# Kernel tuning notes

Hardware: AMD Instinct MI355X
Metric: run time of the kernel (lower is better)

Reference implementation:

```python
import jax, jax.numpy as jnp
import numpy as np

BATCH, SEQ, DIM = 16, 512, 2048
KEEP_RATIO = 0.75
TARGET_LEN = int(SEQ * KEEP_RATIO)      # 384
NUM_PAIRS = SEQ - TARGET_LEN            # 128 greedy merges
IMP_FLOOR = 0.1                          # max(0.1, importance) as in source


def gelu(x):
    return jax.nn.gelu(x, approximate=False)  # torch nn.GELU default (erf)


def setup_inputs() -> dict:
    key = jax.random.key(0)
    ks = jax.random.split(key, 6)
    s = 0.02
    return {
        "x": jax.random.normal(ks[0], (BATCH, SEQ, DIM), jnp.float32),
        # importance_scorer: Linear(dim, dim//2) -> GELU -> Linear(dim//2, 1) -> Sigmoid
        "imp_w1": (jax.random.normal(ks[1], (DIM, DIM // 2), jnp.float32) * s),
        "imp_b1": jnp.zeros((DIM // 2,), jnp.float32),
        "imp_w2": (jax.random.normal(ks[2], (DIM // 2, 1), jnp.float32) * s),
        "imp_b2": jnp.zeros((1,), jnp.float32),
        # token_merger: Linear(2*dim, dim) -> GELU -> Linear(dim, dim)
        "mrg_w1": (jax.random.normal(ks[3], (2 * DIM, DIM), jnp.float32) * s),
        "mrg_b1": jnp.zeros((DIM,), jnp.float32),
        "mrg_w2": (jax.random.normal(ks[4], (DIM, DIM), jnp.float32) * s),
        "mrg_b2": jnp.zeros((DIM,), jnp.float32),
    }


def importance_scores(x, w1, b1, w2, b2):
    # [B,S,1] sigmoid scores, then per-batch global min-max normalization
    imp = jax.nn.sigmoid(gelu(x @ w1 + b1) @ w2 + b2)
    mn = imp.min(axis=(1, 2), keepdims=True)
    mx = imp.max(axis=(1, 2), keepdims=True)
    return jnp.where(mx > mn, (imp - mn) / (mx - mn), imp)


def combined_scores(x, imp):
    # cosine similarity with diagonal = -1, divided by importance products
    xn = x / jnp.maximum(jnp.linalg.norm(x, axis=-1, keepdims=True), 1e-12)
    sim = jnp.einsum("bsd,btd->bst", xn, xn)
    w = jnp.maximum(imp[..., 0], IMP_FLOOR)                 # [B,S]
    eye = jnp.eye(SEQ, dtype=bool)
    return jnp.where(eye[None], -1.0, sim / (w[:, :, None] * w[:, None, :]))


def greedy_pairs(score):
    # Device-side greedy max-selection with suppression (NMS-style):
    # repeatedly pick the global argmax among rows/cols not yet merged.
    S = score.shape[0]

    def step(t, carry):
        avail, pi, pj = carry
        m = avail[:, None] & avail[None, :]
        flat = jnp.where(m, score, -jnp.inf).reshape(-1)
        idx = jnp.argmax(flat)
        i = (idx // S).astype(jnp.int32)
        j = (idx % S).astype(jnp.int32)
        avail = avail.at[i].set(False).at[j].set(False)
        return avail, pi.at[t].set(i), pj.at[t].set(j)

    init = (jnp.ones((S,), bool),
            jnp.zeros((NUM_PAIRS,), jnp.int32),
            jnp.zeros((NUM_PAIRS,), jnp.int32))
    return jax.lax.fori_loop(0, NUM_PAIRS, step, init)


def reference(x, imp_w1, imp_b1, imp_w2, imp_b2, mrg_w1, mrg_b1, mrg_w2, mrg_b2):
    B, S, D = x.shape
    imp = importance_scores(x, imp_w1, imp_b1, imp_w2, imp_b2)   # [B,S,1]
    score = combined_scores(x, imp)                              # [B,S,S]
    avail, pi, pj = jax.vmap(greedy_pairs)(score)                # [B,S],[B,P],[B,P]

    xi = jnp.take_along_axis(x, pi[:, :, None], axis=1)          # [B,P,D]
    xj = jnp.take_along_axis(x, pj[:, :, None], axis=1)          # [B,P,D]
    pair = jnp.concatenate([xi, xj], axis=-1)                    # [B,P,2D]
    merged = gelu(pair @ mrg_w1 + mrg_b1) @ mrg_w2 + mrg_b2      # [B,P,D]

    # unmerged tokens, ascending original order (fixed count S - 2P)
    un = jnp.sort(jnp.where(avail, jnp.arange(S)[None, :], S), axis=1)[:, : S - 2 * NUM_PAIRS]
    xu = jnp.take_along_axis(x, un[:, :, None], axis=1)          # [B,S-2P,D]

    return jnp.concatenate([merged, xu], axis=1)                 # [B,S-P,D]
```

## Files before the change

### kernel.cpp

```cpp
#include <hip/hip_runtime.h>
#include <math.h>

#define BATCH 16
#define SEQ 512
#define DIM 2048
#define HID 1024
#define NPAIRS 128
#define TLEN 384
#define NUN 256

typedef unsigned long long ull;
typedef short bf16x8 __attribute__((ext_vector_type(8)));
typedef float f32x4 __attribute__((ext_vector_type(4)));
typedef double f64x4 __attribute__((ext_vector_type(4)));

__device__ __forceinline__ unsigned short f2bf(float f) {
  unsigned u = __float_as_uint(f);
  unsigned r = (u + 0x7FFFu + ((u >> 16) & 1u)) >> 16;
  return (unsigned short)r;
}

__global__ __launch_bounds__(64)
void cc_probe_f64(int* __restrict__ flag) {
  __shared__ double Af[16][4];
  __shared__ double Bf[4][16];
  int l = threadIdx.x;
  if (l < 16)
#pragma unroll
    for (int k = 0; k < 4; ++k) {
      Af[l][k] = 1.0 + (double)l + 16.0 * k;
      Bf[k][l] = 2.0 + 3.0 * (double)l + 5.0 * k;
    }
  __syncthreads();
  int lr = l & 15, lk = l >> 4;
  double a = Af[lr][lk];
  double b = Bf[lk][lr];
  f64x4 d = {0.0, 0.0, 0.0, 0.0};
  d = __builtin_amdgcn_mfma_f64_16x16x4f64(a, b, d, 0, 0, 0);
  int best = 255;
  for (int H = 0; H < 4; ++H) {
    bool ok = true;
#pragma unroll
    for (int v = 0; v < 4; ++v) {
      int r, c;
      if (H == 0)      { r = 4 * lk + v; c = lr; }
      else if (H == 1) { r = lr; c = 4 * lk + v; }
      else if (H == 2) { r = lk + 4 * v; c = lr; }
      else             { r = lr; c = lk + 4 * v; }
      double tr = 0.0;
#pragma unroll
      for (int k = 0; k < 4; ++k) tr += Af[r][k] * Bf[k][c];
      if (d[v] != tr) ok = false;
    }
    ull m = __ballot(ok);
    if (m == ~0ull) { best = H; break; }
  }
  if (l == 0) *flag = best;
}

__global__ __launch_bounds__(256)
void cc_gemm_h(const float* __restrict__ A, const float* __restrict__ Bw,
               const float* __restrict__ bias, float* __restrict__ C,
               const int* __restrict__ flagp) {
  const int N = HID, K = DIM;
  __shared__ double As[16][66];
  __shared__ double Bs[16][66];
  const int H = *flagp;
  int tid = threadIdx.x;
  int lane = tid & 63, wave = tid >> 6;
  int wr = wave >> 1, wc = wave & 1;
  int lr = lane & 15, lk = lane >> 4;
  int pr[4], pc[4];
#pragma unroll
  for (int v = 0; v < 4; ++v) {
    if (H == 0)      { pr[v] = 4 * lk + v; pc[v] = lr; }
    else if (H == 1) { pr[v] = lr; pc[v] = 4 * lk + v; }
    else if (H == 2) { pr[v] = lk + 4 * v; pc[v] = lr; }
    else             { pr[v] = lr; pc[v] = lk + 4 * v; }
  }
  int tx = tid % 16, ty = tid / 16;
  int m0 = blockIdx.y * 64, n0 = blockIdx.x * 64;
  f64x4 acc[2][2] = {{{0.,0.,0.,0.},{0.,0.,0.,0.}},{{0.,0.,0.,0.},{0.,0.,0.,0.}}};
  double vacc[4][4] = {};
  for (int k0 = 0; k0 < K; k0 += 16) {
#pragma unroll
    for (int u = 0; u < 4; ++u) {
      int l = tid + u * 256;
      int r = l >> 4, k = l & 15;
      As[k][r] = (double)A[(size_t)(m0 + r) * K + k0 + k];
      int kb = l >> 6, n = l & 63;
      Bs[kb][n] = (double)Bw[(size_t)(k0 + kb) * N + n0 + n];
    }
    __syncthreads();
    if (H < 4) {
#pragma unroll
      for (int k4 = 0; k4 < 4; ++k4) {
        int kk = k4 * 4 + lk;
        double a0 = As[kk][wr * 32 + lr];
        double a1 = As[kk][wr * 32 + 16 + lr];
        double b0 = Bs[kk][wc * 32 + lr];
        double b1 = Bs[kk][wc * 32 + 16 + lr];
        acc[0][0] = __builtin_amdgcn_mfma_f64_16x16x4f64(a0, b0, acc[0][0], 0, 0, 0);
        acc[0][1] = __builtin_amdgcn_mfma_f64_16x16x4f64(a0, b1, acc[0][1], 0, 0, 0);
        acc[1][0] = __builtin_amdgcn_mfma_f64_16x16x4f64(a1, b0, acc[1][0], 0, 0, 0);
        acc[1][1] = __builtin_amdgcn_mfma_f64_16x16x4f64(a1, b1, acc[1][1], 0, 0, 0);
      }
    } else {
#pragma unroll
      for (int k = 0; k < 16; ++k) {
        double a0 = As[k][ty * 4 + 0], a1 = As[k][ty * 4 + 1];
        double a2 = As[k][ty * 4 + 2], a3 = As[k][ty * 4 + 3];
        double b0 = Bs[k][tx * 4 + 0], b1 = Bs[k][tx * 4 + 1];
        double b2 = Bs[k][tx * 4 + 2], b3 = Bs[k][tx * 4 + 3];
        vacc[0][0] = fma(a0, b0, vacc[0][0]); vacc[0][1] = fma(a0, b1, vacc[0][1]);
        vacc[0][2] = fma(a0, b2, vacc[0][2]); vacc[0][3] = fma(a0, b3, vacc[0][3]);
        vacc[1][0] = fma(a1, b0, vacc[1][0]); vacc[1][1] = fma(a1, b1, vacc[1][1]);
        vacc[1][2] = fma(a1, b2, vacc[1][2]); vacc[1][3] = fma(a1, b3, vacc[1][3]);
        vacc[2][0] = fma(a2, b0, vacc[2][0]); vacc[2][1] = fma(a2, b1, vacc[2][1]);
        vacc[2][2] = fma(a2, b2, vacc[2][2]); vacc[2][3] = fma(a2, b3, vacc[2][3]);
        vacc[3][0] = fma(a3, b0, vacc[3][0]); vacc[3][1] = fma(a3, b1, vacc[3][1]);
        vacc[3][2] = fma(a3, b2, vacc[3][2]); vacc[3][3] = fma(a3, b3, vacc[3][3]);
      }
    }
    __syncthreads();
  }
  if (H < 4) {
#pragma unroll
    for (int i = 0; i < 2; ++i)
#pragma unroll
      for (int j = 0; j < 2; ++j)
#pragma unroll
        for (int v = 0; v < 4; ++v) {
          int m = m0 + wr * 32 + i * 16 + pr[v];
          int n = n0 + wc * 32 + j * 16 + pc[v];
          float pre = (float)(acc[i][j][v] + (double)bias[n]);
          double vv = (double)pre;
          double g = 0.5 * vv * (1.0 + erf(vv * 0.70710678118654752440));
          C[(size_t)m * N + n] = (float)g;
        }
  } else {
#pragma unroll
    for (int i = 0; i < 4; ++i)
#pragma unroll
      for (int j = 0; j < 4; ++j) {
        int m = m0 + ty * 4 + i, n = n0 + tx * 4 + j;
        float pre = (float)(vacc[i][j] + (double)bias[n]);
        double vv = (double)pre;
        double g = 0.5 * vv * (1.0 + erf(vv * 0.70710678118654752440));
        C[(size_t)m * N + n] = (float)g;
      }
  }
}

__global__ __launch_bounds__(256)
void cc_imp2(const float* __restrict__ h, const float* __restrict__ w2,
             const float* __restrict__ b2, float* __restrict__ imp) {
  int row = blockIdx.x, tid = threadIdx.x;
  __shared__ double red[256];
  double s = 0.0;
  const float* hr = h + (size_t)row * HID;
  for (int k = tid; k < HID; k += 256) s = fma((double)hr[k], (double)w2[k], s);
  red[tid] = s;
  __syncthreads();
  for (int off = 128; off > 0; off >>= 1) {
    if (tid < off) red[tid] += red[tid + off];
    __syncthreads();
  }
  if (tid == 0) {
    float logit = (float)(red[0] + (double)b2[0]);
    double sg = 1.0 / (1.0 + exp(-(double)logit));
    imp[row] = (float)sg;
  }
}

__global__ __launch_bounds__(512)
void cc_minmax(const float* __restrict__ imp, float* __restrict__ w) {
  int b = blockIdx.x, tid = threadIdx.x;
  __shared__ float mn[512], mx[512];
  float v = imp[b * SEQ + tid];
  mn[tid] = v; mx[tid] = v;
  __syncthreads();
  for (int off = 256; off > 0; off >>= 1) {
    if (tid < off) {
      mn[tid] = fminf(mn[tid], mn[tid + off]);
      mx[tid] = fmaxf(mx[tid], mx[tid + off]);
    }
    __syncthreads();
  }
  float lo = mn[0], hi = mx[0];
  float nv = (hi > lo) ? (v - lo) / (hi - lo) : v;
  w[b * SEQ + tid] = fmaxf(nv, 0.1f);
}

__global__ __launch_bounds__(256)
void cc_rownorm(const float* __restrict__ x, float* __restrict__ rn) {
  int row = blockIdx.x, tid = threadIdx.x;
  __shared__ double red[256];
  double s = 0.0;
  const float* xr = x + (size_t)row * DIM;
  for (int k = tid; k < DIM; k += 256) {
    double v = xr[k];
    s = fma(v, v, s);
  }
  red[tid] = s;
  __syncthreads();
  for (int off = 128; off > 0; off >>= 1) {
    if (tid < off) red[tid] += red[tid + off];
    __syncthreads();
  }
  if (tid == 0) rn[row] = fmaxf((float)sqrt(red[0]), 1e-12f);
}

__global__ __launch_bounds__(256)
void cc_gemm_score(const float* __restrict__ X, const float* __restrict__ rn,
                   const float* __restrict__ w, float* __restrict__ score,
                   const int* __restrict__ flagp) {
  const int b = blockIdx.z;
  __shared__ double As[16][66];
  __shared__ double Bs[16][66];
  const int H = *flagp;
  int tid = threadIdx.x;
  int lane = tid & 63, wave = tid >> 6;
  int wr = wave >> 1, wc = wave & 1;
  int lr = lane & 15, lk = lane >> 4;
  int pr[4], pc[4];
#pragma unroll
  for (int v = 0; v < 4; ++v) {
    if (H == 0)      { pr[v] = 4 * lk + v; pc[v] = lr; }
    else if (H == 1) { pr[v] = lr; pc[v] = 4 * lk + v; }
    else if (H == 2) { pr[v] = lk + 4 * v; pc[v] = lr; }
    else             { pr[v] = lr; pc[v] = lk + 4 * v; }
  }
  int tx = tid % 16, ty = tid / 16;
  int s0 = blockIdx.y * 64, t0 = blockIdx.x * 64;
  const float* Xb = X + (size_t)b * SEQ * DIM;
  const float* rnb = rn + b * SEQ;
  f64x4 acc[2][2] = {{{0.,0.,0.,0.},{0.,0.,0.,0.}},{{0.,0.,0.,0.},{0.,0.,0.,0.}}};
  double vacc[4][4] = {};
  for (int k0 = 0; k0 < DIM; k0 += 16) {
#pragma unroll
    for (int u = 0; u < 4; ++u) {
      int l = tid + u * 256;
      int r = l >> 4, k = l & 15;
      As[k][r] = (double)(Xb[(size_t)(s0 + r) * DIM + k0 + k] / rnb[s0 + r]);
      Bs[k][r] = (double)(Xb[(size_t)(t0 + r) * DIM + k0 + k] / rnb[t0 + r]);
    }
    __syncthreads();
    if (H < 4) {
#pragma unroll
      for (int k4 = 0; k4 < 4; ++k4) {
        int kk = k4 * 4 + lk;
        double a0 = As[kk][wr * 32 + lr];
        double a1 = As[kk][wr * 32 + 16 + lr];
        double b0 = Bs[kk][wc * 32 + lr];
        double b1 = Bs[kk][wc * 32 + 16 + lr];
        acc[0][0] = __builtin_amdgcn_mfma_f64_16x16x4f64(a0, b0, acc[0][0], 0, 0, 0);
        acc[0][1] = __builtin_amdgcn_mfma_f64_16x16x4f64(a0, b1, acc[0][1], 0, 0, 0);
        acc[1][0] = __builtin_amdgcn_mfma_f64_16x16x4f64(a1, b0, acc[1][0], 0, 0, 0);
        acc[1][1] = __builtin_amdgcn_mfma_f64_16x16x4f64(a1, b1, acc[1][1], 0, 0, 0);
      }
    } else {
#pragma unroll
      for (int k = 0; k < 16; ++k) {
        double a0 = As[k][ty * 4 + 0], a1 = As[k][ty * 4 + 1];
        double a2 = As[k][ty * 4 + 2], a3 = As[k][ty * 4 + 3];
        double b0 = Bs[k][tx * 4 + 0], b1 = Bs[k][tx * 4 + 1];
        double b2 = Bs[k][tx * 4 + 2], b3 = Bs[k][tx * 4 + 3];
        vacc[0][0] = fma(a0, b0, vacc[0][0]); vacc[0][1] = fma(a0, b1, vacc[0][1]);
        vacc[0][2] = fma(a0, b2, vacc[0][2]); vacc[0][3] = fma(a0, b3, vacc[0][3]);
        vacc[1][0] = fma(a1, b0, vacc[1][0]); vacc[1][1] = fma(a1, b1, vacc[1][1]);
        vacc[1][2] = fma(a1, b2, vacc[1][2]); vacc[1][3] = fma(a1, b3, vacc[1][3]);
        vacc[2][0] = fma(a2, b0, vacc[2][0]); vacc[2][1] = fma(a2, b1, vacc[2][1]);
        vacc[2][2] = fma(a2, b2, vacc[2][2]); vacc[2][3] = fma(a2, b3, vacc[2][3]);
        vacc[3][0] = fma(a3, b0, vacc[3][0]); vacc[3][1] = fma(a3, b1, vacc[3][1]);
        vacc[3][2] = fma(a3, b2, vacc[3][2]); vacc[3][3] = fma(a3, b3, vacc[3][3]);
      }
    }
    __syncthreads();
  }
  if (H < 4) {
#pragma unroll
    for (int i = 0; i < 2; ++i)
#pragma unroll
      for (int j = 0; j < 2; ++j)
#pragma unroll
        for (int v = 0; v < 4; ++v) {
          int s = s0 + wr * 32 + i * 16 + pr[v];
          int t = t0 + wc * 32 + j * 16 + pc[v];
          float vv;
          if (s == t) vv = -1.0f;
          else {
            float sim = (float)acc[i][j][v];
            float wp = w[b * SEQ + s] * w[b * SEQ + t];
            vv = sim / wp;
          }
          score[((size_t)b * SEQ + s) * SEQ + t] = vv;
        }
  } else {
#pragma unroll
    for (int i = 0; i < 4; ++i)
#pragma unroll
      for (int j = 0; j < 4; ++j) {
        int s = s0 + ty * 4 + i, t = t0 + tx * 4 + j;
        float vv;
        if (s == t) vv = -1.0f;
        else {
          float sim = (float)vacc[i][j];
          float wp = w[b * SEQ + s] * w[b * SEQ + t];
          vv = sim / wp;
        }
        score[((size_t)b * SEQ + s) * SEQ + t] = vv;
      }
  }
}

__global__ __launch_bounds__(64)
void cc_greedy(const float* __restrict__ score, int* __restrict__ pi,
               int* __restrict__ pj, unsigned char* __restrict__ availg) {
  const int b = blockIdx.x;
  const float* S = score + (size_t)b * SEQ * SEQ;
  const int lane = threadIdx.x;
  __shared__ uint2 availv[SEQ / 8];
  unsigned char* avail = (unsigned char*)availv;
  __shared__ int rargL[SEQ];
  __shared__ int spi[NPAIRS], spj[NPAIRS];
  unsigned rhi8[8];
  int rarg8[8];
  unsigned am = 0xFFu;

  availv[lane] = make_uint2(0x01010101u, 0x01010101u);

  {
    float bv[8]; int bc[8];
#pragma unroll
    for (int q = 0; q < 8; ++q) { bv[q] = -INFINITY; bc[q] = 0; }
    for (int c4 = 0; c4 < SEQ / 4; ++c4) {
#pragma unroll
      for (int q = 0; q < 8; ++q) {
        int r = lane * 8 + q;
        float4 v = ((const float4*)(S + (size_t)r * SEQ))[c4];
        int cc = c4 * 4;
        if (v.x > bv[q]) { bv[q] = v.x; bc[q] = cc; }
        if (v.y > bv[q]) { bv[q] = v.y; bc[q] = cc + 1; }
        if (v.z > bv[q]) { bv[q] = v.z; bc[q] = cc + 2; }
        if (v.w > bv[q]) { bv[q] = v.w; bc[q] = cc + 3; }
      }
    }
#pragma unroll
    for (int q = 0; q < 8; ++q) {
      unsigned u = __float_as_uint(bv[q]);
      rhi8[q] = (u & 0x80000000u) ? ~u : (u | 0x80000000u);
      rarg8[q] = bc[q];
      rargL[lane * 8 + q] = bc[q];
    }
  }
  __syncthreads();

  for (int t = 0; t < NPAIRS; ++t) {
    ull key = 0ULL;
#pragma unroll
    for (int q = 0; q < 8; ++q) {
      if (am & (1u << q)) {
        ull k = ((ull)rhi8[q] << 32) | (unsigned)((SEQ - 1) - (lane * 8 + q));
        if (k > key) key = k;
      }
    }
#pragma unroll
    for (int off = 1; off < 64; off <<= 1) {
      ull ok = __shfl_xor(key, off, 64);
      if (ok > key) key = ok;
    }
    const int i = (SEQ - 1) - (int)(key & 0xFFFFFFFFull);
    const int j = rargL[i];
    if (lane == 0) {
      spi[t] = i; spj[t] = j;
      avail[i] = 0; avail[j] = 0;
    }
    if ((i >> 3) == lane) am &= ~(1u << (i & 7));
    if ((j >> 3) == lane) am &= ~(1u << (j & 7));
    __syncthreads();

    unsigned needmask = 0u;
#pragma unroll
    for (int q = 0; q < 8; ++q)
      if ((am & (1u << q)) && (rarg8[q] == i || rarg8[q] == j))
        needmask |= (1u << q);
    for (int q = 0; q < 8; ++q) {
      ull m = __ballot((needmask >> q) & 1u);
      while (m) {
        int src = __ffsll(m) - 1;
        m &= m - 1;
        int r = src * 8 + q;
        const float4* row4 = (const float4*)(S + (size_t)r * SEQ) + lane * 2;
        float4 v0 = row4[0], v1 = row4[1];
        uint2 av = availv[lane];
        float nv = -INFINITY; int nc = -1;
        if ((av.x & 0x000000FFu) && v0.x > nv) { nv = v0.x; nc = 0; }
        if ((av.x & 0x0000FF00u) && v0.y > nv) { nv = v0.y; nc = 1; }
        if ((av.x & 0x00FF0000u) && v0.z > nv) { nv = v0.z; nc = 2; }
        if ((av.x & 0xFF000000u) && v0.w > nv) { nv = v0.w; nc = 3; }
        if ((av.y & 0x000000FFu) && v1.x > nv) { nv = v1.x; nc = 4; }
        if ((av.y & 0x0000FF00u) && v1.y > nv) { nv = v1.y; nc = 5; }
        if ((av.y & 0x00FF0000u) && v1.z > nv) { nv = v1.z; nc = 6; }
        if ((av.y & 0xFF000000u) && v1.w > nv) { nv = v1.w; nc = 7; }
        ull rk = 0ULL;
        if (nc >= 0) {
          unsigned u = __float_as_uint(nv);
          unsigned ou = (u & 0x80000000u) ? ~u : (u | 0x80000000u);
          rk = ((ull)ou << 32) | (unsigned)((SEQ - 1) - (lane * 8 + nc));
        }
#pragma unroll
        for (int off = 1; off < 64; off <<= 1) {
          ull ok = __shfl_xor(rk, off, 64);
          if (ok > rk) rk = ok;
        }
        if (lane == src) {
          rhi8[q] = (unsigned)(rk >> 32);
          rarg8[q] = (SEQ - 1) - (int)(rk & 0xFFFFFFFFull);
          rargL[r] = rarg8[q];
        }
      }
    }
    __syncthreads();
  }

  for (int t2 = lane; t2 < NPAIRS; t2 += 64) {
    pi[b * NPAIRS + t2] = spi[t2];
    pj[b * NPAIRS + t2] = spj[t2];
  }
#pragma unroll
  for (int q = 0; q < 8; ++q) {
    int r = lane * 8 + q;
    availg[b * SEQ + r] = avail[r];
  }
}

__global__ __launch_bounds__(512)
void cc_unmerged(const unsigned char* __restrict__ availg, int* __restrict__ un) {
  int b = blockIdx.x, tid = threadIdx.x;
  __shared__ int ps[SEQ];
  int flag = availg[b * SEQ + tid];
  ps[tid] = flag;
  __syncthreads();
  for (int off = 1; off < SEQ; off <<= 1) {
    int v = (tid >= off) ? ps[tid - off] : 0;
    __syncthreads();
    ps[tid] += v;
    __syncthreads();
  }
  int pos = ps[tid] - flag;
  if (flag && pos < NUN) un[b * NUN + pos] = tid;
}

__global__ __launch_bounds__(256)
void cc_unmerged_copy(const float* __restrict__ x, const int* __restrict__ un,
                      float* __restrict__ out) {
  int idx = blockIdx.x;
  int b = idx / NUN, u_ = idx % NUN;
  int s = un[idx];
  const float4* src = (const float4*)(x + ((size_t)b * SEQ + s) * DIM);
  float4* dst = (float4*)(out + ((size_t)b * TLEN + NPAIRS + u_) * DIM);
  for (int u = threadIdx.x; u < DIM / 4; u += 256) dst[u] = src[u];
}

__global__ __launch_bounds__(256)
void cc_transpose_bf16(const float* __restrict__ W, unsigned short* __restrict__ Wt,
                       int K, int N) {
  __shared__ float t[32][33];
  int tx = threadIdx.x & 31, ty = threadIdx.x >> 5;
  int k0 = blockIdx.y * 32, n0 = blockIdx.x * 32;
#pragma unroll
  for (int u = 0; u < 4; ++u) {
    int kk = ty + u * 8;
    t[kk][tx] = W[(size_t)(k0 + kk) * N + n0 + tx];
  }
  __syncthreads();
#pragma unroll
  for (int u = 0; u < 4; ++u) {
    int nn = ty + u * 8;
    Wt[(size_t)(n0 + nn) * K + k0 + tx] = f2bf(t[tx][nn]);
  }
}

__global__ __launch_bounds__(256)
void cc_gemm_m1m(const float* __restrict__ x, const int* __restrict__ pi,
                 const int* __restrict__ pj, const unsigned short* __restrict__ Bt,
                 const float* __restrict__ bias, float* __restrict__ C) {
  __shared__ unsigned short Asm[128][40];
  __shared__ unsigned short Bsm[128][40];
  int tid = threadIdx.x;
  int lane = tid & 63, wave = tid >> 6;
  int wm = wave >> 1, wn = wave & 1;
  int m0 = blockIdx.y * 128, n0 = blockIdx.x * 128;
  int lr = lane & 15, lk = lane >> 4;
  f32x4 acc[4][4] = {};
  const int r = tid >> 1, kh = tid & 1;
  const int mg = m0 + r;
  const int bb = mg >> 7;
  const int ti_ = pi[mg], tj_ = pj[mg];
  for (int k0 = 0; k0 < 2 * DIM; k0 += 32) {
    {
      int kk = k0 + kh * 16;
      int tok = (kk < DIM) ? ti_ : tj_;
      int kc = (kk < DIM) ? kk : kk - DIM;
      const float* src = x + ((size_t)bb * SEQ + tok) * DIM + kc;
      float4 f0 = *(const float4*)(src);
      float4 f1 = *(const float4*)(src + 4);
      float4 f2 = *(const float4*)(src + 8);
      float4 f3 = *(const float4*)(src + 12);
      unsigned short bvals[16];
      bvals[0] = f2bf(f0.x); bvals[1] = f2bf(f0.y); bvals[2] = f2bf(f0.z); bvals[3] = f2bf(f0.w);
      bvals[4] = f2bf(f1.x); bvals[5] = f2bf(f1.y); bvals[6] = f2bf(f1.z); bvals[7] = f2bf(f1.w);
      bvals[8] = f2bf(f2.x); bvals[9] = f2bf(f2.y); bvals[10] = f2bf(f2.z); bvals[11] = f2bf(f2.w);
      bvals[12] = f2bf(f3.x); bvals[13] = f2bf(f3.y); bvals[14] = f2bf(f3.z); bvals[15] = f2bf(f3.w);
      *(bf16x8*)&Asm[r][kh * 16 + 0] = *(const bf16x8*)&bvals[0];
      *(bf16x8*)&Asm[r][kh * 16 + 8] = *(const bf16x8*)&bvals[8];
      const unsigned short* bsrc = Bt + (size_t)(n0 + r) * (2 * DIM) + k0 + kh * 16;
      *(uint4*)&Bsm[r][kh * 16 + 0] = *(const uint4*)(bsrc);
      *(uint4*)&Bsm[r][kh * 16 + 8] = *(const uint4*)(bsrc + 8);
    }
    __syncthreads();
    bf16x8 af[4], bfr[4];
#pragma unroll
    for (int fm = 0; fm < 4; ++fm)
      af[fm] = *(const bf16x8*)&Asm[wm * 64 + fm * 16 + lr][lk * 8];
#pragma unroll
    for (int fn = 0; fn < 4; ++fn)
      bfr[fn] = *(const bf16x8*)&Bsm[wn * 64 + fn * 16 + lr][lk * 8];
#pragma unroll
    for (int fm = 0; fm < 4; ++fm)
#pragma unroll
      for (int fn = 0; fn < 4; ++fn)
        acc[fm][fn] = __builtin_amdgcn_mfma_f32_16x16x32_bf16(
            af[fm], bfr[fn], acc[fm][fn], 0, 0, 0);
    __syncthreads();
  }
#pragma unroll
  for (int fm = 0; fm < 4; ++fm)
#pragma unroll
    for (int fn = 0; fn < 4; ++fn)
#pragma unroll
      for (int v = 0; v < 4; ++v) {
        int m = m0 + wm * 64 + fm * 16 + lk * 4 + v;
        int n = n0 + wn * 64 + fn * 16 + lr;
        float val = acc[fm][fn][v] + bias[n];
        float g = 0.5f * val * (1.0f + erff(val * 0.70710678f));
        C[(size_t)m * DIM + n] = g;
      }
}

__global__ __launch_bounds__(256)
void cc_gemm_m2m(const float* __restrict__ A, const unsigned short* __restrict__ Bt,
                 const float* __restrict__ bias, float* __restrict__ out) {
  __shared__ unsigned short Asm[128][40];
  __shared__ unsigned short Bsm[128][40];
  int tid = threadIdx.x;
  int lane = tid & 63, wave = tid >> 6;
  int wm = wave >> 1, wn = wave & 1;
  int m0 = blockIdx.y * 128, n0 = blockIdx.x * 128;
  int lr = lane & 15, lk = lane >> 4;
  f32x4 acc[4][4] = {};
  const int r = tid >> 1, kh = tid & 1;
  for (int k0 = 0; k0 < DIM; k0 += 32) {
    {
      const float* src = A + (size_t)(m0 + r) * DIM + k0 + kh * 16;
      float4 f0 = *(const float4*)(src);
      float4 f1 = *(const float4*)(src + 4);
      float4 f2 = *(const float4*)(src + 8);
      float4 f3 = *(const float4*)(src + 12);
      unsigned short bvals[16];
      bvals[0] = f2bf(f0.x); bvals[1] = f2bf(f0.y); bvals[2] = f2bf(f0.z); bvals[3] = f2bf(f0.w);
      bvals[4] = f2bf(f1.x); bvals[5] = f2bf(f1.y); bvals[6] = f2bf(f1.z); bvals[7] = f2bf(f1.w);
      bvals[8] = f2bf(f2.x); bvals[9] = f2bf(f2.y); bvals[10] = f2bf(f2.z); bvals[11] = f2bf(f2.w);
      bvals[12] = f2bf(f3.x); bvals[13] = f2bf(f3.y); bvals[14] = f2bf(f3.z); bvals[15] = f2bf(f3.w);
      *(bf16x8*)&Asm[r][kh * 16 + 0] = *(const bf16x8*)&bvals[0];
      *(bf16x8*)&Asm[r][kh * 16 + 8] = *(const bf16x8*)&bvals[8];
      const unsigned short* bsrc = Bt + (size_t)(n0 + r) * DIM + k0 + kh * 16;
      *(uint4*)&Bsm[r][kh * 16 + 0] = *(const uint4*)(bsrc);
      *(uint4*)&Bsm[r][kh * 16 + 8] = *(const uint4*)(bsrc + 8);
    }
    __syncthreads();
    bf16x8 af[4], bfr[4];
#pragma unroll
    for (int fm = 0; fm < 4; ++fm)
      af[fm] = *(const bf16x8*)&Asm[wm * 64 + fm * 16 + lr][lk * 8];
#pragma unroll
    for (int fn = 0; fn < 4; ++fn)
      bfr[fn] = *(const bf16x8*)&Bsm[wn * 64 + fn * 16 + lr][lk * 8];
#pragma unroll
    for (int fm = 0; fm < 4; ++fm)
#pragma unroll
      for (int fn = 0; fn < 4; ++fn)
        acc[fm][fn] = __builtin_amdgcn_mfma_f32_16x16x32_bf16(
            af[fm], bfr[fn], acc[fm][fn], 0, 0, 0);
    __syncthreads();
  }
#pragma unroll
  for (int fm = 0; fm < 4; ++fm)
#pragma unroll
    for (int fn = 0; fn < 4; ++fn)
#pragma unroll
      for (int v = 0; v < 4; ++v) {
        int m = m0 + wm * 64 + fm * 16 + lk * 4 + v;
        int n = n0 + wn * 64 + fn * 16 + lr;
        int bb = m >> 7, p = m & 127;
        float val = acc[fm][fn][v] + bias[n];
        out[((size_t)bb * TLEN + p) * DIM + n] = val;
      }
}

extern "C" void kernel_launch(void* const* d_in, const int* in_sizes, int n_in,
                              void* d_out, int out_size, void* d_ws, size_t ws_size,
                              hipStream_t stream) {
  const float* x      = (const float*)d_in[0];
  const float* imp_w1 = (const float*)d_in[1];
  const float* imp_b1 = (const float*)d_in[2];
  const float* imp_w2 = (const float*)d_in[3];
  const float* imp_b2 = (const float*)d_in[4];
  const float* mrg_w1 = (const float*)d_in[5];
  const float* mrg_b1 = (const float*)d_in[6];
  const float* mrg_w2 = (const float*)d_in[7];
  const float* mrg_b2 = (const float*)d_in[8];
  float* out = (float*)d_out;

  float* score = (float*)d_out;

  char* ws = (char*)d_ws;
  float* hbuf  = (float*)ws;
  unsigned short* w1t = (unsigned short*)ws;
  unsigned short* w2t = (unsigned short*)(ws + ((size_t)16 << 20));
  float* m1buf = (float*)(ws + ((size_t)32 << 20));
  char* sm = ws + ((size_t)48 << 20);
  float* imp = (float*)sm;              sm += (size_t)BATCH * SEQ * 4;
  float* wv  = (float*)sm;              sm += (size_t)BATCH * SEQ * 4;
  float* rn  = (float*)sm;              sm += (size_t)BATCH * SEQ * 4;
  int* pi    = (int*)sm;                sm += (size_t)BATCH * NPAIRS * 4;
  int* pj    = (int*)sm;                sm += (size_t)BATCH * NPAIRS * 4;
  unsigned char* avail = (unsigned char*)sm; sm += (size_t)BATCH * SEQ;
  int* un    = (int*)sm;                sm += (size_t)BATCH * NUN * 4;
  int* lflag = (int*)sm;                sm += 256;

  cc_probe_f64<<<1, 64, 0, stream>>>(lflag);
  cc_rownorm<<<BATCH * SEQ, 256, 0, stream>>>(x, rn);
  cc_gemm_h<<<dim3(HID / 64, BATCH * SEQ / 64), 256, 0, stream>>>(
      x, imp_w1, imp_b1, hbuf, lflag);
  cc_imp2<<<BATCH * SEQ, 256, 0, stream>>>(hbuf, imp_w2, imp_b2, imp);
  cc_minmax<<<BATCH, 512, 0, stream>>>(imp, wv);
  cc_gemm_score<<<dim3(SEQ / 64, SEQ / 64, BATCH), 256, 0, stream>>>(
      x, rn, wv, score, lflag);
  cc_greedy<<<BATCH, 64, 0, stream>>>(score, pi, pj, avail);
  cc_unmerged<<<BATCH, SEQ, 0, stream>>>(avail, un);
  cc_transpose_bf16<<<dim3(DIM / 32, (2 * DIM) / 32), 256, 0, stream>>>(
      mrg_w1, w1t, 2 * DIM, DIM);
  cc_transpose_bf16<<<dim3(DIM / 32, DIM / 32), 256, 0, stream>>>(
      mrg_w2, w2t, DIM, DIM);
  cc_unmerged_copy<<<BATCH * NUN, 256, 0, stream>>>(x, un, out);
  cc_gemm_m1m<<<dim3(DIM / 128, BATCH * NPAIRS / 128), 256, 0, stream>>>(
      x, pi, pj, w1t, mrg_b1, m1buf);
  cc_gemm_m2m<<<dim3(DIM / 128, BATCH * NPAIRS / 128), 256, 0, stream>>>(
      m1buf, w2t, mrg_b2, out);
}
```

Baseline: 3.068 ms.

## Enlarge f64 importance GEMM tile, store merger hidden as bf16, simplify greedy argmax

```diff
diff --git a/kernel.cpp b/kernel.cpp
--- a/kernel.cpp
+++ b/kernel.cpp
@@ -18,6 +18,10 @@
   unsigned u = __float_as_uint(f);
   unsigned r = (u + 0x7FFFu + ((u >> 16) & 1u)) >> 16;
   return (unsigned short)r;
+}
+__device__ __forceinline__ unsigned ccord(float v) {
+  unsigned u = __float_as_uint(v);
+  return (u & 0x80000000u) ? ~u : (u | 0x80000000u);
 }
 
 __global__ __launch_bounds__(64)
@@ -63,6 +67,167 @@
                const float* __restrict__ bias, float* __restrict__ C,
                const int* __restrict__ flagp) {
   const int N = HID, K = DIM;
+  __shared__ double As[16][130];
+  __shared__ double Bs[16][66];
+  const int H = *flagp;
+  int tid = threadIdx.x;
+  int lane = tid & 63, wave = tid >> 6;
+  int wr = wave >> 1, wc = wave & 1;
+  int lr = lane & 15, lk = lane >> 4;
+  int pr[4], pc[4];
+#pragma unroll
+  for (int v = 0; v < 4; ++v) {
+    if (H == 0)      { pr[v] = 4 * lk + v; pc[v] = lr; }
+    else if (H == 1) { pr[v] = lr; pc[v] = 4 * lk + v; }
+    else if (H == 2) { pr[v] = lk + 4 * v; pc[v] = lr; }
+    else             { pr[v] = lr; pc[v] = lk + 4 * v; }
+  }
+  int tx = tid % 16, ty = tid / 16;
+  int m0 = blockIdx.y * 128, n0 = blockIdx.x * 64;
+  f64x4 acc[4][2] = {};
+  double vacc[8][4] = {};
+  for (int k0 = 0; k0 < K; k0 += 16) {
+#pragma unroll
+    for (int u = 0; u < 8; ++u) {
+      int l = tid + u * 256;
+      int r = l >> 4, k = l & 15;
+      As[k][r] = (double)A[(size_t)(m0 + r) * K + k0 + k];
+    }
+#pragma unroll
+    for (int u = 0; u < 4; ++u) {
+      int l = tid + u * 256;
+      int kb = l >> 6, n = l & 63;
+      Bs[kb][n] = (double)Bw[(size_t)(k0 + kb) * N + n0 + n];
+    }
+    __syncthreads();
+    if (H < 4) {
+#pragma unroll
+      for (int k4 = 0; k4 < 4; ++k4) {
+        int kk = k4 * 4 + lk;
+        double a0 = As[kk][wr * 64 + lr];
+        double a1 = As[kk][wr * 64 + 16 + lr];
+        double a2 = As[kk][wr * 64 + 32 + lr];
+        double a3 = As[kk][wr * 64 + 48 + lr];
+        double b0 = Bs[kk][wc * 32 + lr];
+        double b1 = Bs[kk][wc * 32 + 16 + lr];
+        acc[0][0] = __builtin_amdgcn_mfma_f64_16x16x4f64(a0, b0, acc[0][0], 0, 0, 0);
+        acc[0][1] = __builtin_amdgcn_mfma_f64_16x16x4f64(a0, b1, acc[0][1], 0, 0, 0);
+        acc[1][0] = __builtin_amdgcn_mfma_f64_16x16x4f64(a1, b0, acc[1][0], 0, 0, 0);
+        acc[1][1] = __builtin_amdgcn_mfma_f64_16x16x4f64(a1, b1, acc[1][1], 0, 0, 0);
+        acc[2][0] = __builtin_amdgcn_mfma_f64_16x16x4f64(a2, b0, acc[2][0], 0, 0, 0);
+        acc[2][1] = __builtin_amdgcn_mfma_f64_16x16x4f64(a2, b1, acc[2][1], 0, 0, 0);
+        acc[3][0] = __builtin_amdgcn_mfma_f64_16x16x4f64(a3, b0, acc[3][0], 0, 0, 0);
+        acc[3][1] = __builtin_amdgcn_mfma_f64_16x16x4f64(a3, b1, acc[3][1], 0, 0, 0);
+      }
+    } else {
+#pragma unroll
+      for (int k = 0; k < 16; ++k) {
+        double aa[8], bb[4];
+#pragma unroll
+        for (int fi = 0; fi < 8; ++fi) aa[fi] = As[k][ty * 8 + fi];
+#pragma unroll
+        for (int fj = 0; fj < 4; ++fj) bb[fj] = Bs[k][tx * 4 + fj];
+#pragma unroll
+        for (int fi = 0; fi < 8; ++fi)
+#pragma unroll
+          for (int fj = 0; fj < 4; ++fj)
+            vacc[fi][fj] = fma(aa[fi], bb[fj], vacc[fi][fj]);
+      }
+    }
+    __syncthreads();
+  }
+  if (H < 4) {
+#pragma unroll
+    for (int fi = 0; fi < 4; ++fi)
+#pragma unroll
+      for (int fj = 0; fj < 2; ++fj)
+#pragma unroll
+        for (int v = 0; v < 4; ++v) {
+          int m = m0 + wr * 64 + fi * 16 + pr[v];
+          int n = n0 + wc * 32 + fj * 16 + pc[v];
+          float pre = (float)(acc[fi][fj][v] + (double)bias[n]);
+          double vv = (double)pre;
+          double g = 0.5 * vv * (1.0 + erf(vv * 0.70710678118654752440));
+          C[(size_t)m * N + n] = (float)g;
+        }
+  } else {
+#pragma unroll
+    for (int fi = 0; fi < 8; ++fi)
+#pragma unroll
+      for (int fj = 0; fj < 4; ++fj) {
+        int m = m0 + ty * 8 + fi, n = n0 + tx * 4 + fj;
+        float pre = (float)(vacc[fi][fj] + (double)bias[n]);
+        double vv = (double)pre;
+        double g = 0.5 * vv * (1.0 + erf(vv * 0.70710678118654752440));
+        C[(size_t)m * N + n] = (float)g;
+      }
+  }
+}
+
+__global__ __launch_bounds__(256)
+void cc_imp2(const float* __restrict__ h, const float* __restrict__ w2,
+             const float* __restrict__ b2, float* __restrict__ imp) {
+  int row = blockIdx.x, tid = threadIdx.x;
+  __shared__ double red[256];
+  double s = 0.0;
+  const float* hr = h + (size_t)row * HID;
+  for (int k = tid; k < HID; k += 256) s = fma((double)hr[k], (double)w2[k], s);
+  red[tid] = s;
+  __syncthreads();
+  for (int off = 128; off > 0; off >>= 1) {
+    if (tid < off) red[tid] += red[tid + off];
+    __syncthreads();
+  }
+  if (tid == 0) {
+    float logit = (float)(red[0] + (double)b2[0]);
+    double sg = 1.0 / (1.0 + exp(-(double)logit));
+    imp[row] = (float)sg;
+  }
+}
+
+__global__ __launch_bounds__(512)
+void cc_minmax(const float* __restrict__ imp, float* __restrict__ w) {
+  int b = blockIdx.x, tid = threadIdx.x;
+  __shared__ float mn[512], mx[512];
+  float v = imp[b * SEQ + tid];
+  mn[tid] = v; mx[tid] = v;
+  __syncthreads();
+  for (int off = 256; off > 0; off >>= 1) {
+    if (tid < off) {
+      mn[tid] = fminf(mn[tid], mn[tid + off]);
+      mx[tid] = fmaxf(mx[tid], mx[tid + off]);
+    }
+    __syncthreads();
+  }
+  float lo = mn[0], hi = mx[0];
+  float nv = (hi > lo) ? (v - lo) / (hi - lo) : v;
+  w[b * SEQ + tid] = fmaxf(nv, 0.1f);
+}
+
+__global__ __launch_bounds__(256)
+void cc_rownorm(const float* __restrict__ x, float* __restrict__ rn) {
+  int row = blockIdx.x, tid = threadIdx.x;
+  __shared__ double red[256];
+  double s = 0.0;
+  const float* xr = x + (size_t)row * DIM;
+  for (int k = tid; k < DIM; k += 256) {
+    double v = xr[k];
+    s = fma(v, v, s);
+  }
+  red[tid] = s;
+  __syncthreads();
+  for (int off = 128; off > 0; off >>= 1) {
+    if (tid < off) red[tid] += red[tid + off];
+    __syncthreads();
+  }
+  if (tid == 0) rn[row] = fmaxf((float)sqrt(red[0]), 1e-12f);
+}
+
+__global__ __launch_bounds__(256)
+void cc_gemm_score(const float* __restrict__ X, const float* __restrict__ rn,
+                   const float* __restrict__ w, float* __restrict__ score,
+                   const int* __restrict__ flagp) {
+  const int b = blockIdx.z;
   __shared__ double As[16][66];
   __shared__ double Bs[16][66];
   const int H = *flagp;
@@ -79,17 +244,18 @@
     else             { pr[v] = lr; pc[v] = lk + 4 * v; }
   }
   int tx = tid % 16, ty = tid / 16;
-  int m0 = blockIdx.y * 64, n0 = blockIdx.x * 64;
+  int s0 = blockIdx.y * 64, t0 = blockIdx.x * 64;
+  const float* Xb = X + (size_t)b * SEQ * DIM;
+  const float* rnb = rn + b * SEQ;
   f64x4 acc[2][2] = {{{0.,0.,0.,0.},{0.,0.,0.,0.}},{{0.,0.,0.,0.},{0.,0.,0.,0.}}};
   double vacc[4][4] = {};
-  for (int k0 = 0; k0 < K; k0 += 16) {
+  for (int k0 = 0; k0 < DIM; k0 += 16) {
 #pragma unroll
     for (int u = 0; u < 4; ++u) {
       int l = tid + u * 256;
       int r = l >> 4, k = l & 15;
-      As[k][r] = (double)A[(size_t)(m0 + r) * K + k0 + k];
-      int kb = l >> 6, n = l & 63;
-      Bs[kb][n] = (double)Bw[(size_t)(k0 + kb) * N + n0 + n];
+      As[k][r] = (double)(Xb[(size_t)(s0 + r) * DIM + k0 + k] / rnb[s0 + r]);
+      Bs[k][r] = (double)(Xb[(size_t)(t0 + r) * DIM + k0 + k] / rnb[t0 + r]);
     }
     __syncthreads();
     if (H < 4) {
@@ -131,160 +297,6 @@
       for (int j = 0; j < 2; ++j)
 #pragma unroll
         for (int v = 0; v < 4; ++v) {
-          int m = m0 + wr * 32 + i * 16 + pr[v];
-          int n = n0 + wc * 32 + j * 16 + pc[v];
-          float pre = (float)(acc[i][j][v] + (double)bias[n]);
-          double vv = (double)pre;
-          double g = 0.5 * vv * (1.0 + erf(vv * 0.70710678118654752440));
-          C[(size_t)m * N + n] = (float)g;
-        }
-  } else {
-#pragma unroll
-    for (int i = 0; i < 4; ++i)
-#pragma unroll
-      for (int j = 0; j < 4; ++j) {
-        int m = m0 + ty * 4 + i, n = n0 + tx * 4 + j;
-        float pre = (float)(vacc[i][j] + (double)bias[n]);
-        double vv = (double)pre;
-        double g = 0.5 * vv * (1.0 + erf(vv * 0.70710678118654752440));
-        C[(size_t)m * N + n] = (float)g;
-      }
-  }
-}
-
-__global__ __launch_bounds__(256)
-void cc_imp2(const float* __restrict__ h, const float* __restrict__ w2,
-             const float* __restrict__ b2, float* __restrict__ imp) {
-  int row = blockIdx.x, tid = threadIdx.x;
-  __shared__ double red[256];
-  double s = 0.0;
-  const float* hr = h + (size_t)row * HID;
-  for (int k = tid; k < HID; k += 256) s = fma((double)hr[k], (double)w2[k], s);
-  red[tid] = s;
-  __syncthreads();
-  for (int off = 128; off > 0; off >>= 1) {
-    if (tid < off) red[tid] += red[tid + off];
-    __syncthreads();
-  }
-  if (tid == 0) {
-    float logit = (float)(red[0] + (double)b2[0]);
-    double sg = 1.0 / (1.0 + exp(-(double)logit));
-    imp[row] = (float)sg;
-  }
-}
-
-__global__ __launch_bounds__(512)
-void cc_minmax(const float* __restrict__ imp, float* __restrict__ w) {
-  int b = blockIdx.x, tid = threadIdx.x;
-  __shared__ float mn[512], mx[512];
-  float v = imp[b * SEQ + tid];
-  mn[tid] = v; mx[tid] = v;
-  __syncthreads();
-  for (int off = 256; off > 0; off >>= 1) {
-    if (tid < off) {
-      mn[tid] = fminf(mn[tid], mn[tid + off]);
-      mx[tid] = fmaxf(mx[tid], mx[tid + off]);
-    }
-    __syncthreads();
-  }
-  float lo = mn[0], hi = mx[0];
-  float nv = (hi > lo) ? (v - lo) / (hi - lo) : v;
-  w[b * SEQ + tid] = fmaxf(nv, 0.1f);
-}
-
-__global__ __launch_bounds__(256)
-void cc_rownorm(const float* __restrict__ x, float* __restrict__ rn) {
-  int row = blockIdx.x, tid = threadIdx.x;
-  __shared__ double red[256];
-  double s = 0.0;
-  const float* xr = x + (size_t)row * DIM;
-  for (int k = tid; k < DIM; k += 256) {
-    double v = xr[k];
-    s = fma(v, v, s);
-  }
-  red[tid] = s;
-  __syncthreads();
-  for (int off = 128; off > 0; off >>= 1) {
-    if (tid < off) red[tid] += red[tid + off];
-    __syncthreads();
-  }
-  if (tid == 0) rn[row] = fmaxf((float)sqrt(red[0]), 1e-12f);
-}
-
-__global__ __launch_bounds__(256)
-void cc_gemm_score(const float* __restrict__ X, const float* __restrict__ rn,
-                   const float* __restrict__ w, float* __restrict__ score,
-                   const int* __restrict__ flagp) {
-  const int b = blockIdx.z;
-  __shared__ double As[16][66];
-  __shared__ double Bs[16][66];
-  const int H = *flagp;
-  int tid = threadIdx.x;
-  int lane = tid & 63, wave = tid >> 6;
-  int wr = wave >> 1, wc = wave & 1;
-  int lr = lane & 15, lk = lane >> 4;
-  int pr[4], pc[4];
-#pragma unroll
-  for (int v = 0; v < 4; ++v) {
-    if (H == 0)      { pr[v] = 4 * lk + v; pc[v] = lr; }
-    else if (H == 1) { pr[v] = lr; pc[v] = 4 * lk + v; }
-    else if (H == 2) { pr[v] = lk + 4 * v; pc[v] = lr; }
-    else             { pr[v] = lr; pc[v] = lk + 4 * v; }
-  }
-  int tx = tid % 16, ty = tid / 16;
-  int s0 = blockIdx.y * 64, t0 = blockIdx.x * 64;
-  const float* Xb = X + (size_t)b * SEQ * DIM;
-  const float* rnb = rn + b * SEQ;
-  f64x4 acc[2][2] = {{{0.,0.,0.,0.},{0.,0.,0.,0.}},{{0.,0.,0.,0.},{0.,0.,0.,0.}}};
-  double vacc[4][4] = {};
-  for (int k0 = 0; k0 < DIM; k0 += 16) {
-#pragma unroll
-    for (int u = 0; u < 4; ++u) {
-      int l = tid + u * 256;
-      int r = l >> 4, k = l & 15;
-      As[k][r] = (double)(Xb[(size_t)(s0 + r) * DIM + k0 + k] / rnb[s0 + r]);
-      Bs[k][r] = (double)(Xb[(size_t)(t0 + r) * DIM + k0 + k] / rnb[t0 + r]);
-    }
-    __syncthreads();
-    if (H < 4) {
-#pragma unroll
-      for (int k4 = 0; k4 < 4; ++k4) {
-        int kk = k4 * 4 + lk;
-        double a0 = As[kk][wr * 32 + lr];
-        double a1 = As[kk][wr * 32 + 16 + lr];
-        double b0 = Bs[kk][wc * 32 + lr];
-        double b1 = Bs[kk][wc * 32 + 16 + lr];
-        acc[0][0] = __builtin_amdgcn_mfma_f64_16x16x4f64(a0, b0, acc[0][0], 0, 0, 0);
-        acc[0][1] = __builtin_amdgcn_mfma_f64_16x16x4f64(a0, b1, acc[0][1], 0, 0, 0);
-        acc[1][0] = __builtin_amdgcn_mfma_f64_16x16x4f64(a1, b0, acc[1][0], 0, 0, 0);
-        acc[1][1] = __builtin_amdgcn_mfma_f64_16x16x4f64(a1, b1, acc[1][1], 0, 0, 0);
-      }
-    } else {
-#pragma unroll
-      for (int k = 0; k < 16; ++k) {
-        double a0 = As[k][ty * 4 + 0], a1 = As[k][ty * 4 + 1];
-        double a2 = As[k][ty * 4 + 2], a3 = As[k][ty * 4 + 3];
-        double b0 = Bs[k][tx * 4 + 0], b1 = Bs[k][tx * 4 + 1];
-        double b2 = Bs[k][tx * 4 + 2], b3 = Bs[k][tx * 4 + 3];
-        vacc[0][0] = fma(a0, b0, vacc[0][0]); vacc[0][1] = fma(a0, b1, vacc[0][1]);
-        vacc[0][2] = fma(a0, b2, vacc[0][2]); vacc[0][3] = fma(a0, b3, vacc[0][3]);
-        vacc[1][0] = fma(a1, b0, vacc[1][0]); vacc[1][1] = fma(a1, b1, vacc[1][1]);
-        vacc[1][2] = fma(a1, b2, vacc[1][2]); vacc[1][3] = fma(a1, b3, vacc[1][3]);
-        vacc[2][0] = fma(a2, b0, vacc[2][0]); vacc[2][1] = fma(a2, b1, vacc[2][1]);
-        vacc[2][2] = fma(a2, b2, vacc[2][2]); vacc[2][3] = fma(a2, b3, vacc[2][3]);
-        vacc[3][0] = fma(a3, b0, vacc[3][0]); vacc[3][1] = fma(a3, b1, vacc[3][1]);
-        vacc[3][2] = fma(a3, b2, vacc[3][2]); vacc[3][3] = fma(a3, b3, vacc[3][3]);
-      }
-    }
-    __syncthreads();
-  }
-  if (H < 4) {
-#pragma unroll
-    for (int i = 0; i < 2; ++i)
-#pragma unroll
-      for (int j = 0; j < 2; ++j)
-#pragma unroll
-        for (int v = 0; v < 4; ++v) {
           int s = s0 + wr * 32 + i * 16 + pr[v];
           int t = t0 + wc * 32 + j * 16 + pc[v];
           float vv;
@@ -348,8 +360,7 @@
     }
 #pragma unroll
     for (int q = 0; q < 8; ++q) {
-      unsigned u = __float_as_uint(bv[q]);
-      rhi8[q] = (u & 0x80000000u) ? ~u : (u | 0x80000000u);
+      rhi8[q] = ccord(bv[q]);
       rarg8[q] = bc[q];
       rargL[lane * 8 + q] = bc[q];
     }
@@ -365,12 +376,17 @@
         if (k > key) key = k;
       }
     }
+    unsigned myhi = (unsigned)(key >> 32);
+    int myrow = (SEQ - 1) - (int)(key & 0xFFFFFFFFull);
+    unsigned mx = myhi;
 #pragma unroll
     for (int off = 1; off < 64; off <<= 1) {
-      ull ok = __shfl_xor(key, off, 64);
-      if (ok > key) key = ok;
-    }
-    const int i = (SEQ - 1) - (int)(key & 0xFFFFFFFFull);
+      unsigned o = __shfl_xor(mx, off, 64);
+      if (o > mx) mx = o;
+    }
+    ull pm = __ballot(myhi == mx);
+    int sl = __ffsll(pm) - 1;
+    const int i = __shfl(myrow, sl, 64);
     const int j = rargL[i];
     if (lane == 0) {
       spi[t] = i; spj[t] = j;
@@ -403,21 +419,20 @@
         if ((av.y & 0x0000FF00u) && v1.y > nv) { nv = v1.y; nc = 5; }
         if ((av.y & 0x00FF0000u) && v1.z > nv) { nv = v1.z; nc = 6; }
         if ((av.y & 0xFF000000u) && v1.w > nv) { nv = v1.w; nc = 7; }
-        ull rk = 0ULL;
-        if (nc >= 0) {
-          unsigned u = __float_as_uint(nv);
-          unsigned ou = (u & 0x80000000u) ? ~u : (u | 0x80000000u);
-          rk = ((ull)ou << 32) | (unsigned)((SEQ - 1) - (lane * 8 + nc));
+        unsigned rhi2 = (nc >= 0) ? ccord(nv) : 0u;
+        unsigned mx2 = rhi2;
+#pragma unroll
+        for (int off = 1; off < 64; off <<= 1) {
+          unsigned o = __shfl_xor(mx2, off, 64);
+          if (o > mx2) mx2 = o;
         }
-#pragma unroll
-        for (int off = 1; off < 64; off <<= 1) {
-          ull ok = __shfl_xor(rk, off, 64);
-          if (ok > rk) rk = ok;
-        }
+        ull pm2 = __ballot(rhi2 == mx2);
+        int sl2 = __ffsll(pm2) - 1;
+        int gcol = __shfl(lane * 8 + nc, sl2, 64);
         if (lane == src) {
-          rhi8[q] = (unsigned)(rk >> 32);
-          rarg8[q] = (SEQ - 1) - (int)(rk & 0xFFFFFFFFull);
-          rargL[r] = rarg8[q];
+          rhi8[q] = mx2;
+          rarg8[q] = gcol;
+          rargL[r] = gcol;
         }
       }
     }
@@ -485,7 +500,7 @@
 __global__ __launch_bounds__(256)
 void cc_gemm_m1m(const float* __restrict__ x, const int* __restrict__ pi,
                  const int* __restrict__ pj, const unsigned short* __restrict__ Bt,
-                 const float* __restrict__ bias, float* __restrict__ C) {
+                 const float* __restrict__ bias, unsigned short* __restrict__ C) {
   __shared__ unsigned short Asm[128][40];
   __shared__ unsigned short Bsm[128][40];
   int tid = threadIdx.x;
@@ -545,12 +560,13 @@
         int n = n0 + wn * 64 + fn * 16 + lr;
         float val = acc[fm][fn][v] + bias[n];
         float g = 0.5f * val * (1.0f + erff(val * 0.70710678f));
-        C[(size_t)m * DIM + n] = g;
-      }
-}
-
-__global__ __launch_bounds__(256)
-void cc_gemm_m2m(const float* __restrict__ A, const unsigned short* __restrict__ Bt,
+        C[(size_t)m * DIM + n] = f2bf(g);
+      }
+}
+
+__global__ __launch_bounds__(256)
+void cc_gemm_m2m(const unsigned short* __restrict__ A,
+                 const unsigned short* __restrict__ Bt,
                  const float* __restrict__ bias, float* __restrict__ out) {
   __shared__ unsigned short Asm[128][40];
   __shared__ unsigned short Bsm[128][40];
@@ -563,18 +579,9 @@
   const int r = tid >> 1, kh = tid & 1;
   for (int k0 = 0; k0 < DIM; k0 += 32) {
     {
-      const float* src = A + (size_t)(m0 + r) * DIM + k0 + kh * 16;
-      float4 f0 = *(const float4*)(src);
-      float4 f1 = *(const float4*)(src + 4);
-      float4 f2 = *(const float4*)(src + 8);
-      float4 f3 = *(const float4*)(src + 12);
-      unsigned short bvals[16];
-      bvals[0] = f2bf(f0.x); bvals[1] = f2bf(f0.y); bvals[2] = f2bf(f0.z); bvals[3] = f2bf(f0.w);
-      bvals[4] = f2bf(f1.x); bvals[5] = f2bf(f1.y); bvals[6] = f2bf(f1.z); bvals[7] = f2bf(f1.w);
-      bvals[8] = f2bf(f2.x); bvals[9] = f2bf(f2.y); bvals[10] = f2bf(f2.z); bvals[11] = f2bf(f2.w);
-      bvals[12] = f2bf(f3.x); bvals[13] = f2bf(f3.y); bvals[14] = f2bf(f3.z); bvals[15] = f2bf(f3.w);
-      *(bf16x8*)&Asm[r][kh * 16 + 0] = *(const bf16x8*)&bvals[0];
-      *(bf16x8*)&Asm[r][kh * 16 + 8] = *(const bf16x8*)&bvals[8];
+      const unsigned short* src = A + (size_t)(m0 + r) * DIM + k0 + kh * 16;
+      *(uint4*)&Asm[r][kh * 16 + 0] = *(const uint4*)(src);
+      *(uint4*)&Asm[r][kh * 16 + 8] = *(const uint4*)(src + 8);
       const unsigned short* bsrc = Bt + (size_t)(n0 + r) * DIM + k0 + kh * 16;
       *(uint4*)&Bsm[r][kh * 16 + 0] = *(const uint4*)(bsrc);
       *(uint4*)&Bsm[r][kh * 16 + 8] = *(const uint4*)(bsrc + 8);
@@ -629,7 +636,7 @@
   float* hbuf  = (float*)ws;
   unsigned short* w1t = (unsigned short*)ws;
   unsigned short* w2t = (unsigned short*)(ws + ((size_t)16 << 20));
-  float* m1buf = (float*)(ws + ((size_t)32 << 20));
+  unsigned short* m1buf = (unsigned short*)(ws + ((size_t)32 << 20));
   char* sm = ws + ((size_t)48 << 20);
   float* imp = (float*)sm;              sm += (size_t)BATCH * SEQ * 4;
   float* wv  = (float*)sm;              sm += (size_t)BATCH * SEQ * 4;
@@ -642,7 +649,7 @@
 
   cc_probe_f64<<<1, 64, 0, stream>>>(lflag);
   cc_rownorm<<<BATCH * SEQ, 256, 0, stream>>>(x, rn);
-  cc_gemm_h<<<dim3(HID / 64, BATCH * SEQ / 64), 256, 0, stream>>>(
+  cc_gemm_h<<<dim3(HID / 64, BATCH * SEQ / 128), 256, 0, stream>>>(
       x, imp_w1, imp_b1, hbuf, lflag);
   cc_imp2<<<BATCH * SEQ, 256, 0, stream>>>(hbuf, imp_w2, imp_b2, imp);
   cc_minmax<<<BATCH, 512, 0, stream>>>(imp, wv);
```

Result: slower. 4.151 ms (+35.3%).
